# Optimization experiments

Measured on AMD Instinct MI355X. Metric: run time of the kernel, lower is better.

## Reference

```python
import jax, jax.numpy as jnp
import numpy as np
from jax import lax

B, INP, OUP, H, W = 16, 128, 128, 56, 56
EXPAND = 6
HID = INP * EXPAND  # 768
EPS = 1e-5


def setup_inputs() -> dict:
    key = jax.random.key(0)
    ks = jax.random.split(key, 18)
    x = jax.random.normal(ks[0], (B, INP, H, W), dtype=jnp.float32)
    mask = jax.random.randint(ks[1], (B, 1, H, W), 0, 2, dtype=jnp.int32)
    w1 = jax.random.normal(ks[2], (HID, INP), dtype=jnp.float32) * 0.05
    g1 = 1.0 + 0.1 * jax.random.normal(ks[3], (HID,), dtype=jnp.float32)
    b1 = 0.1 * jax.random.normal(ks[4], (HID,), dtype=jnp.float32)
    m1 = 0.1 * jax.random.normal(ks[5], (HID,), dtype=jnp.float32)
    v1 = jax.random.uniform(ks[6], (HID,), dtype=jnp.float32) + 0.5
    wdw = jax.random.normal(ks[7], (HID, 1, 3, 3), dtype=jnp.float32) * 0.05
    g2 = 1.0 + 0.1 * jax.random.normal(ks[8], (HID,), dtype=jnp.float32)
    b2 = 0.1 * jax.random.normal(ks[9], (HID,), dtype=jnp.float32)
    m2 = 0.1 * jax.random.normal(ks[10], (HID,), dtype=jnp.float32)
    v2 = jax.random.uniform(ks[11], (HID,), dtype=jnp.float32) + 0.5
    w2 = jax.random.normal(ks[12], (OUP, HID), dtype=jnp.float32) * 0.05
    g3 = 1.0 + 0.1 * jax.random.normal(ks[13], (OUP,), dtype=jnp.float32)
    b3 = 0.1 * jax.random.normal(ks[14], (OUP,), dtype=jnp.float32)
    m3 = 0.1 * jax.random.normal(ks[15], (OUP,), dtype=jnp.float32)
    v3 = jax.random.uniform(ks[16], (OUP,), dtype=jnp.float32) + 0.5
    return dict(x=x, w1=w1, g1=g1, b1=b1, m1=m1, v1=v1, wdw=wdw,
                g2=g2, b2=b2, m2=m2, v2=v2, w2=w2,
                g3=g3, b3=b3, m3=m3, v3=v3, mask=mask)


def _bn(h, g, b, m, v):
    # inference-mode BatchNorm2d: (h - mean) * gamma/sqrt(var+eps) + beta
    scale = g / jnp.sqrt(v + EPS)
    return (h - m[None, :, None, None]) * scale[None, :, None, None] + b[None, :, None, None]


def reference(x, w1, g1, b1, m1, v1, wdw, g2, b2, m2, v2, w2, g3, b3, m3, v3, mask):
    mf = mask.astype(x.dtype)  # [B,1,H,W] binary mask ('std')
    # mask_dilate: 3x3 binary dilation (dilate_stride=1) so the depthwise conv
    # has valid neighbors for every active output pixel
    md = lax.reduce_window(mf, 0.0, lax.max, (1, 1, 3, 3), (1, 1, 1, 1), 'SAME')
    # expand 1x1 conv + BN + ReLU6, restricted to dilated mask
    h = jnp.einsum('bchw,kc->bkhw', x, w1)            # [B,HID,H,W]
    h = jnp.clip(_bn(h, g1, b1, m1, v1), 0.0, 6.0) * md
    # depthwise 3x3 conv + BN + ReLU6, restricted to std mask
    h = lax.conv_general_dilated(h, wdw, (1, 1), 'SAME',
                                 feature_group_count=HID,
                                 dimension_numbers=('NCHW', 'OIHW', 'NCHW'))
    h = jnp.clip(_bn(h, g2, b2, m2, v2), 0.0, 6.0) * mf
    # project 1x1 conv + BN (no relu), restricted to std mask
    h = jnp.einsum('bkhw,ok->bohw', h, w2)            # [B,OUP,H,W]
    h = _bn(h, g3, b3, m3, v3) * mf
    # scatter-add into identity path
    return x + h
```

## Files before the change

### kernel.cpp

```cpp
#include <hip/hip_runtime.h>
#include <hip/hip_bf16.h>

#define BATCH 16
#define INP   128
#define OUP   128
#define HH    56
#define WW    56
#define HWSZ  3136
#define HID   768
#define EPSV  1e-5f

#define SCPD  62
#define ROWD  (32 * SCPD)
#define H2STR 72

typedef __attribute__((ext_vector_type(8))) short bf16x8;
typedef __attribute__((ext_vector_type(4))) float f32x4;

__device__ __forceinline__ unsigned short f2b(float f) {
    unsigned u = __float_as_uint(f);
    return (unsigned short)((u + 0x7FFFu + ((u >> 16) & 1u)) >> 16);
}
__device__ __forceinline__ unsigned pkbf(float lo, float hi) {
    unsigned r;
    asm("v_cvt_pk_bf16_f32 %0, %1, %2" : "=v"(r) : "v"(lo), "v"(hi));
    return r;
}

__global__ void prep(const float* __restrict__ w1, const float* __restrict__ g1,
                     const float* __restrict__ b1, const float* __restrict__ m1, const float* __restrict__ v1,
                     const float* __restrict__ wdw, const float* __restrict__ g2,
                     const float* __restrict__ b2, const float* __restrict__ m2, const float* __restrict__ v2,
                     const float* __restrict__ w2, const float* __restrict__ g3,
                     const float* __restrict__ b3, const float* __restrict__ m3, const float* __restrict__ v3,
                     const int* __restrict__ mask,
                     unsigned short* __restrict__ w1f, unsigned short* __restrict__ w2f,
                     float* __restrict__ be1o, float* __restrict__ wdsf,
                     float* __restrict__ be2o, float* __restrict__ be3o,
                     float* __restrict__ mdf, float* __restrict__ mff)
{
    int gid = blockIdx.x * blockDim.x + threadIdx.x;
    int stp = gridDim.x * blockDim.x;
    for (int i = gid; i < HID * INP; i += stp) {
        int r = i >> 7, k = i & 127;
        float s = g1[r] * rsqrtf(v1[r] + EPSV);
        int ht = r >> 4, r16 = r & 15, ks = k >> 5, g = (k >> 3) & 3, e = k & 7;
        w1f[((((ht * 4 + ks) * 4 + g) * 16 + r16) << 3) + e] = f2b(w1[i] * s);
    }
    for (int i = gid; i < OUP * HID; i += stp) {
        int r = i / HID, k = i - r * HID;
        float s = g3[r] * rsqrtf(v3[r] + EPSV);
        int ot = r >> 4, r16 = r & 15, ch = k >> 6, ks = (k >> 5) & 1, g = (k >> 3) & 3, e = k & 7;
        int lane = g * 16 + r16;
        w2f[((((ot * 12 + ch) * 2 + ks) * 64 + lane) << 3) + e] = f2b(w2[i] * s);
    }
    for (int i = gid; i < HID; i += stp) {
        float s1 = g1[i] * rsqrtf(v1[i] + EPSV);
        be1o[i] = b1[i] - m1[i] * s1;
        float s2 = g2[i] * rsqrtf(v2[i] + EPSV);
        be2o[i] = b2[i] - m2[i] * s2;
    }
    for (int i = gid; i < HID * 9; i += stp) {
        int q = i / HID, c = i - q * HID;
        float s2 = g2[c] * rsqrtf(v2[c] + EPSV);
        wdsf[i] = wdw[c * 9 + q] * s2;
    }
    for (int i = gid; i < OUP; i += stp) {
        float s3 = g3[i] * rsqrtf(v3[i] + EPSV);
        be3o[i] = b3[i] - m3[i] * s3;
    }
    for (int i = gid; i < BATCH * HWSZ; i += stp) {
        int b = i / HWSZ, p = i - b * HWSZ;
        int y = p / WW, xx = p - y * WW;
        float mf = (float)mask[i];
        float md = 0.f;
        for (int dy = -1; dy <= 1; ++dy)
            for (int dx = -1; dx <= 1; ++dx) {
                int yy = y + dy, xc = xx + dx;
                if (yy >= 0 && yy < HH && xc >= 0 && xc < WW)
                    md = fmaxf(md, (float)mask[b * HWSZ + yy * WW + xc]);
            }
        mff[i] = mf;
        mdf[i] = md;
    }
}

__launch_bounds__(512, 4)
__global__ void k1_expand(const float* __restrict__ x,
                          const unsigned short* __restrict__ w1f,
                          const float* __restrict__ be1g,
                          const float* __restrict__ mdf,
                          unsigned* __restrict__ h1p)
{
    __shared__ unsigned short xs[128 * 128];
    const int t = threadIdx.x, lane = t & 63, wv = t >> 6;
    const int g = lane >> 4, r16 = lane & 15;
    const int pid = blockIdx.x;
    const int l = (pid & 7) * 150 + (pid >> 3);
    const int hb = l % 3;
    const int pb = (l / 3) % 25;
    const int b  = l / 75;
    const int p0 = pb * 128;
    const int whid = wv & 3;
    const int wpx  = wv >> 2;

    for (int rep = 0; rep < 8; ++rep) {
        int id = t + rep * 512;
        int px = id & 127, c4 = id >> 7;
        int p = p0 + px;
        ushort4 u; u.x = 0; u.y = 0; u.z = 0; u.w = 0;
        if (p < HWSZ) {
            const float* xp = x + ((size_t)(b * INP + c4 * 4)) * HWSZ + p;
            unsigned lo = pkbf(xp[0], xp[HWSZ]);
            unsigned hi = pkbf(xp[2 * HWSZ], xp[3 * HWSZ]);
            u.x = (unsigned short)lo; u.y = (unsigned short)(lo >> 16);
            u.z = (unsigned short)hi; u.w = (unsigned short)(hi >> 16);
        }
        *(ushort4*)&xs[px * 128 + (((c4 >> 1) ^ (px & 15)) << 3) + ((c4 & 1) << 2)] = u;
    }
    __syncthreads();

    f32x4 acc[4][4];
    #pragma unroll
    for (int mt = 0; mt < 4; ++mt)
        #pragma unroll
        for (int nt = 0; nt < 4; ++nt) {
            acc[mt][nt][0] = 0.f; acc[mt][nt][1] = 0.f;
            acc[mt][nt][2] = 0.f; acc[mt][nt][3] = 0.f;
        }
    const int hbase = hb * 256 + whid * 64;
    const int htb = hbase >> 4;

    #pragma unroll
    for (int ks = 0; ks < 4; ++ks) {
        bf16x8 af[4];
        #pragma unroll
        for (int mt = 0; mt < 4; ++mt)
            af[mt] = *(const bf16x8*)&w1f[((((htb + mt) * 4 + ks) * 64) + lane) << 3];
        #pragma unroll
        for (int nt = 0; nt < 4; ++nt) {
            int px = wpx * 64 + nt * 16 + r16;
            bf16x8 bf = *(const bf16x8*)&xs[px * 128 + (((ks * 4 + g) ^ r16) << 3)];
            #pragma unroll
            for (int mt = 0; mt < 4; ++mt)
                acc[mt][nt] = __builtin_amdgcn_mfma_f32_16x16x32_bf16(af[mt], bf, acc[mt][nt], 0, 0, 0);
        }
    }

    #pragma unroll
    for (int nt = 0; nt < 4; ++nt) {
        const int pg = p0 + wpx * 64 + nt * 16;
        if (pg >= HWSZ) continue;
        const int p = pg + r16;
        const float md = mdf[b * HWSZ + p];
        #pragma unroll
        for (int mt = 0; mt < 4; ++mt) {
            const float4 be4 = *(const float4*)&be1g[hbase + mt * 16 + g * 4];
            f32x4 a = acc[mt][nt];
            float v0 = fminf(fmaxf(a[0] + be4.x, 0.f), 6.f) * md;
            float v1 = fminf(fmaxf(a[1] + be4.y, 0.f), 6.f) * md;
            float v2 = fminf(fmaxf(a[2] + be4.z, 0.f), 6.f) * md;
            float v3 = fminf(fmaxf(a[3] + be4.w, 0.f), 6.f) * md;
            const int c2 = (hbase >> 1) + mt * 8 + g * 2;
            const size_t ad = (size_t)(b * 384 + c2) * HWSZ + p;
            h1p[ad] = pkbf(v0, v1);
            h1p[ad + HWSZ] = pkbf(v2, v3);
        }
    }
}

__launch_bounds__(512, 4)
__global__ void k23(const unsigned* __restrict__ h1p,
                    const unsigned short* __restrict__ w2f,
                    const float* __restrict__ wdsf,
                    const float* __restrict__ be2g,
                    const float* __restrict__ be3g,
                    const float* __restrict__ mff,
                    const float* __restrict__ x,
                    float* __restrict__ out)
{
    __shared__ unsigned stg[4 * ROWD];
    __shared__ unsigned short h2s[112 * H2STR];
    __shared__ float mfv_[112];

    const int t = threadIdx.x, lane = t & 63, wv = t >> 6;
    const int g = lane >> 4, r16 = lane & 15;
    const int pid = blockIdx.x;
    const int l = (pid & 7) * 56 + (pid >> 3);
    const int strip = l % 28, b = l / 28;
    const int y0 = strip * 2, p0 = strip * 112;

    if (t < 112) mfv_[t] = mff[b * HWSZ + p0 + t];
    if (t < 256) {
        int cp = t & 31, rs = (t >> 5) & 3, side = t >> 7;
        stg[rs * ROWD + cp * SCPD + (side ? 58 : 1)] = 0;
    }

    unsigned gaddr[4]; int laddr[4]; bool gval[4], wval[4];
    #pragma unroll
    for (int rep = 0; rep < 4; ++rep) {
        const int id = t + rep * 512;
        const int rr  = (id * 4682) >> 16;
        const int px4 = id - rr * 14;
        const int row = rr & 3, cp = rr >> 2;
        const int gy = y0 - 1 + row;
        wval[rep] = id < 1792;
        gval[rep] = wval[rep] && gy >= 0 && gy < HH;
        gaddr[rep] = (unsigned)((b * 384 + cp) * HWSZ + gy * WW + px4 * 4);
        laddr[rep] = row * ROWD + cp * SCPD + 2 + px4 * 4;
    }
    uint4 sreg[4];

    auto issueLoads = [&]() {
        #pragma unroll
        for (int rep = 0; rep < 4; ++rep) {
            uint4 u; u.x = 0; u.y = 0; u.z = 0; u.w = 0;
            if (gval[rep]) u = *(const uint4*)&h1p[gaddr[rep]];
            sreg[rep] = u;
            gaddr[rep] += 32 * HWSZ;
        }
    };
    auto stageWrite = [&]() {
        #pragma unroll
        for (int rep = 0; rep < 4; ++rep) {
            if (wval[rep]) {
                unsigned* s = &stg[laddr[rep]];
                uint2 a; a.x = sreg[rep].x; a.y = sreg[rep].y;
                uint2 c; c.x = sreg[rep].z; c.y = sreg[rep].w;
                *(uint2*)(s) = a;
                *(uint2*)(s + 2) = c;
            }
        }
    };

    const int c = lane, row2 = (t >> 6) & 1, q = t >> 7;
    const int cp_dw = c >> 1;
    const int shl = (c & 1) ? 0 : 16;
    const unsigned* dwbase = &stg[cp_dw * SCPD + 2 + q * 14];

    auto phaseDW = [&](int ch) {
        float wt[9];
        #pragma unroll
        for (int q9 = 0; q9 < 9; ++q9) wt[q9] = wdsf[q9 * HID + ch * 64 + c];
        const float be = be2g[ch * 64 + c];
        float acc[14];
        #pragma unroll
        for (int j = 0; j < 14; ++j) acc[j] = be;
        #pragma unroll
        for (int dy = 0; dy < 3; ++dy) {
            const unsigned* rp = dwbase + (row2 + dy) * ROWD;
            unsigned uw[16];
            uw[0] = rp[-1];
            #pragma unroll
            for (int i = 0; i < 7; ++i) {
                uint2 d = *(const uint2*)(rp + 2 * i);
                uw[1 + 2 * i] = d.x; uw[2 + 2 * i] = d.y;
            }
            uw[15] = rp[14];
            float fl[16];
            #pragma unroll
            for (int i = 0; i < 16; ++i)
                fl[i] = __uint_as_float((uw[i] << shl) & 0xFFFF0000u);
            #pragma unroll
            for (int j = 0; j < 14; ++j)
                acc[j] += fl[j] * wt[dy * 3] + fl[j + 1] * wt[dy * 3 + 1] + fl[j + 2] * wt[dy * 3 + 2];
        }
        #pragma unroll
        for (int j = 0; j < 14; ++j) {
            const int px = row2 * 56 + q * 14 + j;
            const float mv = mfv_[px];
            float v = fminf(fmaxf(acc[j], 0.f), 6.f) * mv;
            h2s[px * H2STR + (((c >> 3) ^ (px & 7)) << 3) + (c & 7)] = (unsigned short)pkbf(v, v);
        }
    };

    f32x4 pacc[7];
    #pragma unroll
    for (int nt = 0; nt < 7; ++nt) {
        pacc[nt][0] = 0.f; pacc[nt][1] = 0.f; pacc[nt][2] = 0.f; pacc[nt][3] = 0.f;
    }

    auto phaseP = [&](int ch) {
        #pragma unroll
        for (int ks = 0; ks < 2; ++ks) {
            const bf16x8 pw = *(const bf16x8*)&w2f[((((wv * 12 + ch) * 2 + ks) * 64) + lane) << 3];
            #pragma unroll
            for (int nt = 0; nt < 7; ++nt) {
                const int px = nt * 16 + r16;
                const bf16x8 hb = *(const bf16x8*)&h2s[px * H2STR + (((ks * 4 + g) ^ (px & 7)) << 3)];
                pacc[nt] = __builtin_amdgcn_mfma_f32_16x16x32_bf16(pw, hb, pacc[nt], 0, 0, 0);
            }
        }
    };

    issueLoads();
    stageWrite();
    __syncthreads();
    for (int ch = 0; ch < 12; ++ch) {
        if (ch + 1 < 12) issueLoads();
        phaseDW(ch);
        __syncthreads();
        if (ch + 1 < 12) stageWrite();
        phaseP(ch);
        __syncthreads();
    }

    {
        const int ob = wv * 16 + g * 4;
        const float4 be4 = *(const float4*)&be3g[ob];
        #pragma unroll
        for (int nt = 0; nt < 7; ++nt) {
            const int px = nt * 16 + r16;
            const float mv = mfv_[px];
            const size_t base = (size_t)(b * OUP + ob) * HWSZ + p0 + px;
            out[base]            = x[base]            + (pacc[nt][0] + be4.x) * mv;
            out[base + HWSZ]     = x[base + HWSZ]     + (pacc[nt][1] + be4.y) * mv;
            out[base + 2 * HWSZ] = x[base + 2 * HWSZ] + (pacc[nt][2] + be4.z) * mv;
            out[base + 3 * HWSZ] = x[base + 3 * HWSZ] + (pacc[nt][3] + be4.w) * mv;
        }
    }
}

extern "C" void kernel_launch(void* const* d_in, const int* in_sizes, int n_in,
                              void* d_out, int out_size, void* d_ws, size_t ws_size,
                              hipStream_t stream) {
    (void)in_sizes; (void)n_in; (void)out_size; (void)ws_size;
    const float* x   = (const float*)d_in[0];
    const float* w1  = (const float*)d_in[1];
    const float* g1  = (const float*)d_in[2];
    const float* b1  = (const float*)d_in[3];
    const float* m1  = (const float*)d_in[4];
    const float* v1  = (const float*)d_in[5];
    const float* wdw = (const float*)d_in[6];
    const float* g2  = (const float*)d_in[7];
    const float* b2  = (const float*)d_in[8];
    const float* m2  = (const float*)d_in[9];
    const float* v2  = (const float*)d_in[10];
    const float* w2  = (const float*)d_in[11];
    const float* g3  = (const float*)d_in[12];
    const float* b3  = (const float*)d_in[13];
    const float* m3  = (const float*)d_in[14];
    const float* v3  = (const float*)d_in[15];
    const int*  mask = (const int*)d_in[16];
    float* out = (float*)d_out;

    char* ws = (char*)d_ws;
    unsigned short* w1f = (unsigned short*)ws;
    unsigned short* w2f = (unsigned short*)(ws + 196608);
    float* be1o = (float*)(ws + 393216);
    float* wdsf = (float*)(ws + 396288);
    float* be2o = (float*)(ws + 423936);
    float* be3o = (float*)(ws + 427008);
    float* mdf  = (float*)(ws + 427520);
    float* mff  = (float*)(ws + 628224);
    unsigned* h1p = (unsigned*)(ws + 828928);

    prep<<<256, 256, 0, stream>>>(w1, g1, b1, m1, v1, wdw, g2, b2, m2, v2,
                                  w2, g3, b3, m3, v3, mask,
                                  w1f, w2f, be1o, wdsf, be2o, be3o, mdf, mff);
    k1_expand<<<dim3(1200), 512, 0, stream>>>(x, w1f, be1o, mdf, h1p);
    k23<<<dim3(448), 512, 0, stream>>>(h1p, w2f, wdsf, be2o, be3o, mff, x, out);
}
```

Baseline: 92.08 us.

## Retile expand and fused dw/project kernels into smaller tiles with more blocks

k1_expand now processes 64-pixel tiles and loops over all three hidden-channel blocks inside one block, so x is loaded and converted once per tile instead of three times. k23 splits each two-row strip into two half-width segments of 28 columns, which doubles the grid to 896 blocks for better CU occupancy and shrinks shared memory. It also skips the depthwise output conversion where the mask is zero and uses fmed3 for the clamp. The cost is wasted MFMA work on padded pixels (56 of 64 valid), plus extra halo loads and edge handling in k23.

Result: slower. 106.4 us (+15.5%).

```diff
diff --git a/kernel.cpp b/kernel.cpp
--- a/kernel.cpp
+++ b/kernel.cpp
@@ -10,8 +10,7 @@
 #define HID   768
 #define EPSV  1e-5f
 
-#define SCPD  62
-#define ROWD  (32 * SCPD)
+#define SCPW  146
 #define H2STR 72
 
 typedef __attribute__((ext_vector_type(8))) short bf16x8;
@@ -92,79 +91,78 @@
                           const float* __restrict__ mdf,
                           unsigned* __restrict__ h1p)
 {
-    __shared__ unsigned short xs[128 * 128];
+    __shared__ unsigned short xs[64 * 128];
     const int t = threadIdx.x, lane = t & 63, wv = t >> 6;
     const int g = lane >> 4, r16 = lane & 15;
     const int pid = blockIdx.x;
-    const int l = (pid & 7) * 150 + (pid >> 3);
-    const int hb = l % 3;
-    const int pb = (l / 3) % 25;
-    const int b  = l / 75;
-    const int p0 = pb * 128;
+    const int l = (pid & 7) * 98 + (pid >> 3);
+    const int tile = l % 49;
+    const int b    = l / 49;
+    const int p0 = tile * 64;
     const int whid = wv & 3;
     const int wpx  = wv >> 2;
 
-    for (int rep = 0; rep < 8; ++rep) {
+    #pragma unroll
+    for (int rep = 0; rep < 4; ++rep) {
         int id = t + rep * 512;
-        int px = id & 127, c4 = id >> 7;
+        int px = id & 63, c4 = id >> 6;
         int p = p0 + px;
-        ushort4 u; u.x = 0; u.y = 0; u.z = 0; u.w = 0;
-        if (p < HWSZ) {
-            const float* xp = x + ((size_t)(b * INP + c4 * 4)) * HWSZ + p;
-            unsigned lo = pkbf(xp[0], xp[HWSZ]);
-            unsigned hi = pkbf(xp[2 * HWSZ], xp[3 * HWSZ]);
-            u.x = (unsigned short)lo; u.y = (unsigned short)(lo >> 16);
-            u.z = (unsigned short)hi; u.w = (unsigned short)(hi >> 16);
-        }
+        const float* xp = x + ((size_t)(b * INP + c4 * 4)) * HWSZ + p;
+        unsigned lo = pkbf(xp[0], xp[HWSZ]);
+        unsigned hi = pkbf(xp[2 * HWSZ], xp[3 * HWSZ]);
+        ushort4 u;
+        u.x = (unsigned short)lo; u.y = (unsigned short)(lo >> 16);
+        u.z = (unsigned short)hi; u.w = (unsigned short)(hi >> 16);
         *(ushort4*)&xs[px * 128 + (((c4 >> 1) ^ (px & 15)) << 3) + ((c4 & 1) << 2)] = u;
     }
     __syncthreads();
 
-    f32x4 acc[4][4];
-    #pragma unroll
-    for (int mt = 0; mt < 4; ++mt)
-        #pragma unroll
-        for (int nt = 0; nt < 4; ++nt) {
-            acc[mt][nt][0] = 0.f; acc[mt][nt][1] = 0.f;
-            acc[mt][nt][2] = 0.f; acc[mt][nt][3] = 0.f;
-        }
-    const int hbase = hb * 256 + whid * 64;
-    const int htb = hbase >> 4;
-
-    #pragma unroll
-    for (int ks = 0; ks < 4; ++ks) {
-        bf16x8 af[4];
+    #pragma unroll 1
+    for (int hb = 0; hb < 3; ++hb) {
+        f32x4 acc[4][2];
         #pragma unroll
         for (int mt = 0; mt < 4; ++mt)
-            af[mt] = *(const bf16x8*)&w1f[((((htb + mt) * 4 + ks) * 64) + lane) << 3];
-        #pragma unroll
-        for (int nt = 0; nt < 4; ++nt) {
-            int px = wpx * 64 + nt * 16 + r16;
-            bf16x8 bf = *(const bf16x8*)&xs[px * 128 + (((ks * 4 + g) ^ r16) << 3)];
+            #pragma unroll
+            for (int nt = 0; nt < 2; ++nt) {
+                acc[mt][nt][0] = 0.f; acc[mt][nt][1] = 0.f;
+                acc[mt][nt][2] = 0.f; acc[mt][nt][3] = 0.f;
+            }
+        const int hbase = hb * 256 + whid * 64;
+        const int htb = hbase >> 4;
+
+        #pragma unroll
+        for (int ks = 0; ks < 4; ++ks) {
+            bf16x8 af[4];
             #pragma unroll
             for (int mt = 0; mt < 4; ++mt)
-                acc[mt][nt] = __builtin_amdgcn_mfma_f32_16x16x32_bf16(af[mt], bf, acc[mt][nt], 0, 0, 0);
-        }
-    }
-
-    #pragma unroll
-    for (int nt = 0; nt < 4; ++nt) {
-        const int pg = p0 + wpx * 64 + nt * 16;
-        if (pg >= HWSZ) continue;
-        const int p = pg + r16;
-        const float md = mdf[b * HWSZ + p];
-        #pragma unroll
-        for (int mt = 0; mt < 4; ++mt) {
-            const float4 be4 = *(const float4*)&be1g[hbase + mt * 16 + g * 4];
-            f32x4 a = acc[mt][nt];
-            float v0 = fminf(fmaxf(a[0] + be4.x, 0.f), 6.f) * md;
-            float v1 = fminf(fmaxf(a[1] + be4.y, 0.f), 6.f) * md;
-            float v2 = fminf(fmaxf(a[2] + be4.z, 0.f), 6.f) * md;
-            float v3 = fminf(fmaxf(a[3] + be4.w, 0.f), 6.f) * md;
-            const int c2 = (hbase >> 1) + mt * 8 + g * 2;
-            const size_t ad = (size_t)(b * 384 + c2) * HWSZ + p;
-            h1p[ad] = pkbf(v0, v1);
-            h1p[ad + HWSZ] = pkbf(v2, v3);
+                af[mt] = *(const bf16x8*)&w1f[((((htb + mt) * 4 + ks) * 64) + lane) << 3];
+            #pragma unroll
+            for (int nt = 0; nt < 2; ++nt) {
+                int px = wpx * 32 + nt * 16 + r16;
+                bf16x8 bf = *(const bf16x8*)&xs[px * 128 + (((ks * 4 + g) ^ r16) << 3)];
+                #pragma unroll
+                for (int mt = 0; mt < 4; ++mt)
+                    acc[mt][nt] = __builtin_amdgcn_mfma_f32_16x16x32_bf16(af[mt], bf, acc[mt][nt], 0, 0, 0);
+            }
+        }
+
+        #pragma unroll
+        for (int nt = 0; nt < 2; ++nt) {
+            const int p = p0 + wpx * 32 + nt * 16 + r16;
+            const float md = mdf[b * HWSZ + p];
+            #pragma unroll
+            for (int mt = 0; mt < 4; ++mt) {
+                const float4 be4 = *(const float4*)&be1g[hbase + mt * 16 + g * 4];
+                f32x4 a = acc[mt][nt];
+                float v0 = fminf(fmaxf(a[0] + be4.x, 0.f), 6.f) * md;
+                float v1 = fminf(fmaxf(a[1] + be4.y, 0.f), 6.f) * md;
+                float v2 = fminf(fmaxf(a[2] + be4.z, 0.f), 6.f) * md;
+                float v3 = fminf(fmaxf(a[3] + be4.w, 0.f), 6.f) * md;
+                const int c2 = (hbase >> 1) + mt * 8 + g * 2;
+                const size_t ad = (size_t)(b * 384 + c2) * HWSZ + p;
+                h1p[ad] = pkbf(v0, v1);
+                h1p[ad + HWSZ] = pkbf(v2, v3);
+            }
         }
     }
 }
@@ -179,41 +177,46 @@
                     const float* __restrict__ x,
                     float* __restrict__ out)
 {
-    __shared__ unsigned stg[4 * ROWD];
-    __shared__ unsigned short h2s[112 * H2STR];
-    __shared__ float mfv_[112];
+    __shared__ unsigned stg[32 * SCPW];
+    __shared__ unsigned short h2s[64 * H2STR];
+    __shared__ float mfv_[56];
 
     const int t = threadIdx.x, lane = t & 63, wv = t >> 6;
     const int g = lane >> 4, r16 = lane & 15;
     const int pid = blockIdx.x;
-    const int l = (pid & 7) * 56 + (pid >> 3);
-    const int strip = l % 28, b = l / 28;
-    const int y0 = strip * 2, p0 = strip * 112;
-
-    if (t < 112) mfv_[t] = mff[b * HWSZ + p0 + t];
-    if (t < 256) {
-        int cp = t & 31, rs = (t >> 5) & 3, side = t >> 7;
-        stg[rs * ROWD + cp * SCPD + (side ? 58 : 1)] = 0;
-    }
-
-    unsigned gaddr[4]; int laddr[4]; bool gval[4], wval[4];
+    const int l = (pid & 7) * 112 + (pid >> 3);
+    const int seg = l % 56, b = l / 56;
+    const int strip = seg >> 1, xh = seg & 1;
+    const int y0 = strip * 2, x0 = xh * 28;
+
+    if (t < 56) {
+        int row = t >= 28 ? 1 : 0, xx = t - row * 28;
+        mfv_[t] = mff[b * HWSZ + (y0 + row) * WW + x0 + xx];
+    }
+    {
+        unsigned* h2d = (unsigned*)h2s;
+        if (t < 288) h2d[56 * 36 + t] = 0;
+    }
+
+    int gaddr[3], laddr[3]; bool gval[3], wval[3];
     #pragma unroll
-    for (int rep = 0; rep < 4; ++rep) {
+    for (int rep = 0; rep < 3; ++rep) {
         const int id = t + rep * 512;
-        const int rr  = (id * 4682) >> 16;
-        const int px4 = id - rr * 14;
-        const int row = rr & 3, cp = rr >> 2;
+        const int quad = id % 9;
+        const int rc = id / 9;
+        const int row = rc & 3, cp = rc >> 2;
         const int gy = y0 - 1 + row;
-        wval[rep] = id < 1792;
-        gval[rep] = wval[rep] && gy >= 0 && gy < HH;
-        gaddr[rep] = (unsigned)((b * 384 + cp) * HWSZ + gy * WW + px4 * 4);
-        laddr[rep] = row * ROWD + cp * SCPD + 2 + px4 * 4;
-    }
-    uint4 sreg[4];
+        const int gx = x0 - 4 + quad * 4;
+        wval[rep] = id < 1152;
+        gval[rep] = wval[rep] && gy >= 0 && gy < HH && gx >= 0 && gx <= WW - 4;
+        gaddr[rep] = (b * 384 + cp) * HWSZ + gy * WW + gx;
+        laddr[rep] = cp * SCPW + row * 36 + quad * 4;
+    }
+    uint4 sreg[3];
 
     auto issueLoads = [&]() {
         #pragma unroll
-        for (int rep = 0; rep < 4; ++rep) {
+        for (int rep = 0; rep < 3; ++rep) {
             uint4 u; u.x = 0; u.y = 0; u.z = 0; u.w = 0;
             if (gval[rep]) u = *(const uint4*)&h1p[gaddr[rep]];
             sreg[rep] = u;
@@ -222,7 +225,7 @@
     };
     auto stageWrite = [&]() {
         #pragma unroll
-        for (int rep = 0; rep < 4; ++rep) {
+        for (int rep = 0; rep < 3; ++rep) {
             if (wval[rep]) {
                 unsigned* s = &stg[laddr[rep]];
                 uint2 a; a.x = sreg[rep].x; a.y = sreg[rep].y;
@@ -236,47 +239,41 @@
     const int c = lane, row2 = (t >> 6) & 1, q = t >> 7;
     const int cp_dw = c >> 1;
     const int shl = (c & 1) ? 0 : 16;
-    const unsigned* dwbase = &stg[cp_dw * SCPD + 2 + q * 14];
+    const unsigned* dwbase = &stg[cp_dw * SCPW + 3 + q * 7];
 
     auto phaseDW = [&](int ch) {
         float wt[9];
         #pragma unroll
         for (int q9 = 0; q9 < 9; ++q9) wt[q9] = wdsf[q9 * HID + ch * 64 + c];
         const float be = be2g[ch * 64 + c];
-        float acc[14];
-        #pragma unroll
-        for (int j = 0; j < 14; ++j) acc[j] = be;
+        float acc[7];
+        #pragma unroll
+        for (int j = 0; j < 7; ++j) acc[j] = be;
         #pragma unroll
         for (int dy = 0; dy < 3; ++dy) {
-            const unsigned* rp = dwbase + (row2 + dy) * ROWD;
-            unsigned uw[16];
-            uw[0] = rp[-1];
-            #pragma unroll
-            for (int i = 0; i < 7; ++i) {
-                uint2 d = *(const uint2*)(rp + 2 * i);
-                uw[1 + 2 * i] = d.x; uw[2 + 2 * i] = d.y;
-            }
-            uw[15] = rp[14];
-            float fl[16];
-            #pragma unroll
-            for (int i = 0; i < 16; ++i)
-                fl[i] = __uint_as_float((uw[i] << shl) & 0xFFFF0000u);
-            #pragma unroll
-            for (int j = 0; j < 14; ++j)
+            const unsigned* rp = dwbase + (row2 + dy) * 36;
+            float fl[9];
+            #pragma unroll
+            for (int k = 0; k < 9; ++k)
+                fl[k] = __uint_as_float((rp[k] << shl) & 0xFFFF0000u);
+            #pragma unroll
+            for (int j = 0; j < 7; ++j)
                 acc[j] += fl[j] * wt[dy * 3] + fl[j + 1] * wt[dy * 3 + 1] + fl[j + 2] * wt[dy * 3 + 2];
         }
         #pragma unroll
-        for (int j = 0; j < 14; ++j) {
-            const int px = row2 * 56 + q * 14 + j;
+        for (int j = 0; j < 7; ++j) {
+            const int px = row2 * 28 + q * 7 + j;
             const float mv = mfv_[px];
-            float v = fminf(fmaxf(acc[j], 0.f), 6.f) * mv;
-            h2s[px * H2STR + (((c >> 3) ^ (px & 7)) << 3) + (c & 7)] = (unsigned short)pkbf(v, v);
+            unsigned short hv = 0;
+            if (mv != 0.f)
+                hv = (unsigned short)pkbf(__builtin_amdgcn_fmed3f(acc[j], 0.f, 6.f), 0.f);
+            h2s[px * H2STR + (((c >> 3) ^ (px & 7)) << 3) + (c & 7)] = hv;
         }
     };
 
-    f32x4 pacc[7];
+    f32x4 pacc[4];
     #pragma unroll
-    for (int nt = 0; nt < 7; ++nt) {
+    for (int nt = 0; nt < 4; ++nt) {
         pacc[nt][0] = 0.f; pacc[nt][1] = 0.f; pacc[nt][2] = 0.f; pacc[nt][3] = 0.f;
     }
 
@@ -285,7 +282,7 @@
         for (int ks = 0; ks < 2; ++ks) {
             const bf16x8 pw = *(const bf16x8*)&w2f[((((wv * 12 + ch) * 2 + ks) * 64) + lane) << 3];
             #pragma unroll
-            for (int nt = 0; nt < 7; ++nt) {
+            for (int nt = 0; nt < 4; ++nt) {
                 const int px = nt * 16 + r16;
                 const bf16x8 hb = *(const bf16x8*)&h2s[px * H2STR + (((ks * 4 + g) ^ (px & 7)) << 3)];
                 pacc[nt] = __builtin_amdgcn_mfma_f32_16x16x32_bf16(pw, hb, pacc[nt], 0, 0, 0);
@@ -309,14 +306,18 @@
         const int ob = wv * 16 + g * 4;
         const float4 be4 = *(const float4*)&be3g[ob];
         #pragma unroll
-        for (int nt = 0; nt < 7; ++nt) {
+        for (int nt = 0; nt < 4; ++nt) {
             const int px = nt * 16 + r16;
-            const float mv = mfv_[px];
-            const size_t base = (size_t)(b * OUP + ob) * HWSZ + p0 + px;
-            out[base]            = x[base]            + (pacc[nt][0] + be4.x) * mv;
-            out[base + HWSZ]     = x[base + HWSZ]     + (pacc[nt][1] + be4.y) * mv;
-            out[base + 2 * HWSZ] = x[base + 2 * HWSZ] + (pacc[nt][2] + be4.z) * mv;
-            out[base + 3 * HWSZ] = x[base + 3 * HWSZ] + (pacc[nt][3] + be4.w) * mv;
+            if (px < 56) {
+                const int row = px >= 28 ? 1 : 0;
+                const int xx = px - row * 28;
+                const float mv = mfv_[px];
+                const size_t base = (size_t)(b * OUP + ob) * HWSZ + (y0 + row) * WW + x0 + xx;
+                out[base]            = x[base]            + (pacc[nt][0] + be4.x) * mv;
+                out[base + HWSZ]     = x[base + HWSZ]     + (pacc[nt][1] + be4.y) * mv;
+                out[base + 2 * HWSZ] = x[base + 2 * HWSZ] + (pacc[nt][2] + be4.z) * mv;
+                out[base + 3 * HWSZ] = x[base + 3 * HWSZ] + (pacc[nt][3] + be4.w) * mv;
+            }
         }
     }
 }
@@ -358,6 +359,6 @@
     prep<<<256, 256, 0, stream>>>(w1, g1, b1, m1, v1, wdw, g2, b2, m2, v2,
                                   w2, g3, b3, m3, v3, mask,
                                   w1f, w2f, be1o, wdsf, be2o, be3o, mdf, mff);
-    k1_expand<<<dim3(1200), 512, 0, stream>>>(x, w1f, be1o, mdf, h1p);
-    k23<<<dim3(448), 512, 0, stream>>>(h1p, w2f, wdsf, be2o, be3o, mff, x, out);
-}
+    k1_expand<<<dim3(784), 512, 0, stream>>>(x, w1f, be1o, mdf, h1p);
+    k23<<<dim3(896), 512, 0, stream>>>(h1p, w2f, wdsf, be2o, be3o, mff, x, out);
+}
```

## Split k23 into producer and consumer warps with 1024-thread blocks

Applied to the files above, without the earlier changes.

Doubles the k23 block size to 1024 threads. The upper 512 threads act as producers that issue the global loads and write the staging buffer, while the lower 512 do the depthwise conv. Each depthwise thread now handles a bf16 channel pair, decoding both halves of one packed word, so the old shift-based selection is gone. The projection MFMA work is split across 16 waves, each owning 4 pixel tiles. The aim is to overlap memory traffic with compute and raise parallelism, at the cost of more barrier participants, idle waves in some phases, and possibly lower occupancy from register limits under the 1024 launch bound.

After: 207.9 us. 2.26x slower.

```diff
diff --git a/kernel.cpp b/kernel.cpp
--- a/kernel.cpp
+++ b/kernel.cpp
@@ -10,8 +10,7 @@
 #define HID   768
 #define EPSV  1e-5f
 
-#define SCPD  62
-#define ROWD  (32 * SCPD)
+#define RWST  1992
 #define H2STR 72
 
 typedef __attribute__((ext_vector_type(8))) short bf16x8;
@@ -21,6 +20,8 @@
     unsigned u = __float_as_uint(f);
     return (unsigned short)((u + 0x7FFFu + ((u >> 16) & 1u)) >> 16);
 }
+__device__ __forceinline__ float blo(unsigned u){ return __uint_as_float(u << 16); }
+__device__ __forceinline__ float bhi(unsigned u){ return __uint_as_float(u & 0xFFFF0000u); }
 __device__ __forceinline__ unsigned pkbf(float lo, float hi) {
     unsigned r;
     asm("v_cvt_pk_bf16_f32 %0, %1, %2" : "=v"(r) : "v"(lo), "v"(hi));
@@ -169,7 +170,7 @@
     }
 }
 
-__launch_bounds__(512, 4)
+__launch_bounds__(1024, 8)
 __global__ void k23(const unsigned* __restrict__ h1p,
                     const unsigned short* __restrict__ w2f,
                     const float* __restrict__ wdsf,
@@ -179,11 +180,13 @@
                     const float* __restrict__ x,
                     float* __restrict__ out)
 {
-    __shared__ unsigned stg[4 * ROWD];
+    __shared__ unsigned stg[4 * RWST];
     __shared__ unsigned short h2s[112 * H2STR];
     __shared__ float mfv_[112];
 
-    const int t = threadIdx.x, lane = t & 63, wv = t >> 6;
+    const int t = threadIdx.x, lane = t & 63;
+    const int wvid = t >> 6;
+    const bool producer = t >= 512;
     const int g = lane >> 4, r16 = lane & 15;
     const int pid = blockIdx.x;
     const int l = (pid & 7) * 56 + (pid >> 3);
@@ -191,25 +194,28 @@
     const int y0 = strip * 2, p0 = strip * 112;
 
     if (t < 112) mfv_[t] = mff[b * HWSZ + p0 + t];
-    if (t < 256) {
-        int cp = t & 31, rs = (t >> 5) & 3, side = t >> 7;
-        stg[rs * ROWD + cp * SCPD + (side ? 58 : 1)] = 0;
-    }
-
-    unsigned gaddr[4]; int laddr[4]; bool gval[4], wval[4];
-    #pragma unroll
-    for (int rep = 0; rep < 4; ++rep) {
-        const int id = t + rep * 512;
-        const int rr  = (id * 4682) >> 16;
-        const int px4 = id - rr * 14;
-        const int row = rr & 3, cp = rr >> 2;
-        const int gy = y0 - 1 + row;
-        wval[rep] = id < 1792;
-        gval[rep] = wval[rep] && gy >= 0 && gy < HH;
-        gaddr[rep] = (unsigned)((b * 384 + cp) * HWSZ + gy * WW + px4 * 4);
-        laddr[rep] = row * ROWD + cp * SCPD + 2 + px4 * 4;
-    }
+    if (t >= 112 && t < 368) {
+        int i = t - 112;
+        int cp = i & 31, rs = (i >> 5) & 3, side = (i >> 7) & 1;
+        stg[rs * RWST + cp * 62 + (side ? 58 : 1)] = 0;
+    }
+
+    int gaddr[4], laddr[4]; bool gval[4], wval[4];
     uint4 sreg[4];
+    if (producer) {
+        #pragma unroll
+        for (int rep = 0; rep < 4; ++rep) {
+            const int id = (t - 512) + rep * 512;
+            const int rr  = (id * 4682) >> 16;
+            const int px4 = id - rr * 14;
+            const int row = rr & 3, cp = rr >> 2;
+            const int gy = y0 - 1 + row;
+            wval[rep] = id < 1792;
+            gval[rep] = wval[rep] && gy >= 0 && gy < HH;
+            gaddr[rep] = (b * 384 + cp) * HWSZ + gy * WW + px4 * 4;
+            laddr[rep] = row * RWST + cp * 62 + 2 + px4 * 4;
+        }
+    }
 
     auto issueLoads = [&]() {
         #pragma unroll
@@ -233,90 +239,95 @@
         }
     };
 
-    const int c = lane, row2 = (t >> 6) & 1, q = t >> 7;
-    const int cp_dw = c >> 1;
-    const int shl = (c & 1) ? 0 : 16;
-    const unsigned* dwbase = &stg[cp_dw * SCPD + 2 + q * 14];
+    const int cp_c = t & 31, row2 = (t >> 5) & 1, q = (t >> 6) & 7;
+    unsigned* const h2d = (unsigned*)h2s;
 
     auto phaseDW = [&](int ch) {
-        float wt[9];
-        #pragma unroll
-        for (int q9 = 0; q9 < 9; ++q9) wt[q9] = wdsf[q9 * HID + ch * 64 + c];
-        const float be = be2g[ch * 64 + c];
-        float acc[14];
-        #pragma unroll
-        for (int j = 0; j < 14; ++j) acc[j] = be;
+        const float2 be2 = *(const float2*)&be2g[ch * 64 + 2 * cp_c];
+        float accL[7], accH[7];
+        #pragma unroll
+        for (int j = 0; j < 7; ++j) { accL[j] = be2.x; accH[j] = be2.y; }
         #pragma unroll
         for (int dy = 0; dy < 3; ++dy) {
-            const unsigned* rp = dwbase + (row2 + dy) * ROWD;
-            unsigned uw[16];
-            uw[0] = rp[-1];
+            const float2 w0 = *(const float2*)&wdsf[(dy * 3 + 0) * HID + ch * 64 + 2 * cp_c];
+            const float2 w1 = *(const float2*)&wdsf[(dy * 3 + 1) * HID + ch * 64 + 2 * cp_c];
+            const float2 w2 = *(const float2*)&wdsf[(dy * 3 + 2) * HID + ch * 64 + 2 * cp_c];
+            const unsigned* rp = &stg[(row2 + dy) * RWST + cp_c * 62 + 1 + q * 7];
+            float pL[9], pH[9];
             #pragma unroll
-            for (int i = 0; i < 7; ++i) {
-                uint2 d = *(const uint2*)(rp + 2 * i);
-                uw[1 + 2 * i] = d.x; uw[2 + 2 * i] = d.y;
-            }
-            uw[15] = rp[14];
-            float fl[16];
+            for (int k = 0; k < 9; ++k) {
+                unsigned u = rp[k];
+                pL[k] = blo(u); pH[k] = bhi(u);
+            }
             #pragma unroll
-            for (int i = 0; i < 16; ++i)
-                fl[i] = __uint_as_float((uw[i] << shl) & 0xFFFF0000u);
+            for (int j = 0; j < 7; ++j) {
+                accL[j] += pL[j] * w0.x + pL[j + 1] * w1.x + pL[j + 2] * w2.x;
+                accH[j] += pH[j] * w0.y + pH[j + 1] * w1.y + pH[j + 2] * w2.y;
+            }
+        }
+        #pragma unroll
+        for (int j = 0; j < 7; ++j) {
+            const int px = row2 * 56 + q * 7 + j;
+            const float mv = mfv_[px];
+            float vL = fminf(fmaxf(accL[j], 0.f), 6.f) * mv;
+            float vH = fminf(fmaxf(accH[j], 0.f), 6.f) * mv;
+            h2d[px * 36 + (((cp_c >> 2) ^ (px & 7)) << 2) + (cp_c & 3)] = pkbf(vL, vH);
+        }
+    };
+
+    const int ot = wvid >> 1;
+    const int nt0 = (wvid & 1) * 4;
+    f32x4 pacc[4];
+    #pragma unroll
+    for (int i = 0; i < 4; ++i) {
+        pacc[i][0] = 0.f; pacc[i][1] = 0.f; pacc[i][2] = 0.f; pacc[i][3] = 0.f;
+    }
+
+    auto phaseP = [&](int ch) {
+        #pragma unroll
+        for (int ks = 0; ks < 2; ++ks) {
+            const bf16x8 pw = *(const bf16x8*)&w2f[((((ot * 12 + ch) * 2 + ks) * 64) + lane) << 3];
             #pragma unroll
-            for (int j = 0; j < 14; ++j)
-                acc[j] += fl[j] * wt[dy * 3] + fl[j + 1] * wt[dy * 3 + 1] + fl[j + 2] * wt[dy * 3 + 2];
-        }
-        #pragma unroll
-        for (int j = 0; j < 14; ++j) {
-            const int px = row2 * 56 + q * 14 + j;
-            const float mv = mfv_[px];
-            float v = fminf(fmaxf(acc[j], 0.f), 6.f) * mv;
-            h2s[px * H2STR + (((c >> 3) ^ (px & 7)) << 3) + (c & 7)] = (unsigned short)pkbf(v, v);
+            for (int i = 0; i < 4; ++i) {
+                const int nt = nt0 + i;
+                if (nt < 7) {
+                    const int px = nt * 16 + r16;
+                    const bf16x8 hb = *(const bf16x8*)&h2s[px * H2STR + (((ks * 4 + g) ^ (px & 7)) << 3)];
+                    pacc[i] = __builtin_amdgcn_mfma_f32_16x16x32_bf16(pw, hb, pacc[i], 0, 0, 0);
+                }
+            }
         }
     };
 
-    f32x4 pacc[7];
-    #pragma unroll
-    for (int nt = 0; nt < 7; ++nt) {
-        pacc[nt][0] = 0.f; pacc[nt][1] = 0.f; pacc[nt][2] = 0.f; pacc[nt][3] = 0.f;
-    }
-
-    auto phaseP = [&](int ch) {
-        #pragma unroll
-        for (int ks = 0; ks < 2; ++ks) {
-            const bf16x8 pw = *(const bf16x8*)&w2f[((((wv * 12 + ch) * 2 + ks) * 64) + lane) << 3];
-            #pragma unroll
-            for (int nt = 0; nt < 7; ++nt) {
-                const int px = nt * 16 + r16;
-                const bf16x8 hb = *(const bf16x8*)&h2s[px * H2STR + (((ks * 4 + g) ^ (px & 7)) << 3)];
-                pacc[nt] = __builtin_amdgcn_mfma_f32_16x16x32_bf16(pw, hb, pacc[nt], 0, 0, 0);
-            }
-        }
-    };
-
-    issueLoads();
-    stageWrite();
+    if (producer) { issueLoads(); stageWrite(); }
     __syncthreads();
     for (int ch = 0; ch < 12; ++ch) {
-        if (ch + 1 < 12) issueLoads();
-        phaseDW(ch);
+        if (producer) {
+            if (ch + 1 < 12) issueLoads();
+        } else {
+            phaseDW(ch);
+        }
         __syncthreads();
-        if (ch + 1 < 12) stageWrite();
+        if (producer && ch + 1 < 12) stageWrite();
         phaseP(ch);
         __syncthreads();
     }
 
     {
-        const int ob = wv * 16 + g * 4;
+        const int ob = ot * 16 + g * 4;
         const float4 be4 = *(const float4*)&be3g[ob];
         #pragma unroll
-        for (int nt = 0; nt < 7; ++nt) {
-            const int px = nt * 16 + r16;
-            const float mv = mfv_[px];
-            const size_t base = (size_t)(b * OUP + ob) * HWSZ + p0 + px;
-            out[base]            = x[base]            + (pacc[nt][0] + be4.x) * mv;
-            out[base + HWSZ]     = x[base + HWSZ]     + (pacc[nt][1] + be4.y) * mv;
-            out[base + 2 * HWSZ] = x[base + 2 * HWSZ] + (pacc[nt][2] + be4.z) * mv;
-            out[base + 3 * HWSZ] = x[base + 3 * HWSZ] + (pacc[nt][3] + be4.w) * mv;
+        for (int i = 0; i < 4; ++i) {
+            const int nt = nt0 + i;
+            if (nt < 7) {
+                const int px = nt * 16 + r16;
+                const float mv = mfv_[px];
+                const size_t base = (size_t)(b * OUP + ob) * HWSZ + p0 + px;
+                out[base]            = x[base]            + (pacc[i][0] + be4.x) * mv;
+                out[base + HWSZ]     = x[base + HWSZ]     + (pacc[i][1] + be4.y) * mv;
+                out[base + 2 * HWSZ] = x[base + 2 * HWSZ] + (pacc[i][2] + be4.z) * mv;
+                out[base + 3 * HWSZ] = x[base + 3 * HWSZ] + (pacc[i][3] + be4.w) * mv;
+            }
         }
     }
 }
@@ -359,5 +370,5 @@
                                   w2, g3, b3, m3, v3, mask,
                                   w1f, w2f, be1o, wdsf, be2o, be3o, mdf, mff);
     k1_expand<<<dim3(1200), 512, 0, stream>>>(x, w1f, be1o, mdf, h1p);
-    k23<<<dim3(448), 512, 0, stream>>>(h1p, w2f, wdsf, be2o, be3o, mff, x, out);
-}
+    k23<<<dim3(448), 1024, 0, stream>>>(h1p, w2f, wdsf, be2o, be3o, mff, x, out);
+}
```
